# Performance work log

Measured on AMD Instinct MI355X. Metric: run time of the kernel, lower is better.

## Reference

```python
import jax, jax.numpy as jnp
import numpy as np
from math import sqrt


def setup_inputs() -> dict:
    key = jax.random.key(0)
    k1, k2, k3, k4, k5 = jax.random.split(key, 5)
    B, L, H, D = 16, 4096, 16, 64
    S, M = 4096, 256
    queries = jax.random.normal(k1, (B, L, H, D), dtype=jnp.float32)
    keys = jax.random.normal(k2, (B, S, H, D), dtype=jnp.float32)
    values = jax.random.normal(k3, (B, S, H, D), dtype=jnp.float32)
    # nn.Linear(L_k=S, M): weight [M, S], bias [M]
    squeeze_w = jax.random.normal(k4, (M, S), dtype=jnp.float32) / sqrt(S)
    squeeze_b = jax.random.normal(k5, (M,), dtype=jnp.float32) * 0.01
    return {"queries": queries, "keys": keys, "values": values,
            "squeeze_w": squeeze_w, "squeeze_b": squeeze_b}


def reference(queries, keys, values, squeeze_w, squeeze_b):
    # queries: [B,L,H,D]; keys/values: [B,S,H,D]; squeeze_w: [M,S]; squeeze_b: [M]
    B, L, H, D = queries.shape
    scale = 1.0 / sqrt(D)
    bias = squeeze_b[None, :, None, None]  # broadcast over [B,M,H,D]
    # Linear over the sequence axis S -> M (Linformer compression)
    keys_sq = jnp.einsum('bshd,ms->bmhd', keys, squeeze_w) + bias      # [B,M,H,D]
    values_sq = jnp.einsum('bshd,ms->bmhd', values, squeeze_w) + bias  # [B,M,H,D]
    # Scaled dot-product attention against compressed K/V
    attn = jnp.einsum('blhd,bmhd->bhlm', queries, keys_sq) * scale     # [B,H,L,M]
    attn = jax.nn.softmax(attn, axis=-1)  # dropout is identity in eval / p=0
    context = jnp.einsum('bhlm,bmhd->blhd', attn, values_sq)           # [B,L,H,D]
    return context
```

## Files before the change

kernel.cpp:

```cpp
#include <hip/hip_runtime.h>

#define NB 16
#define NL 4096
#define NH 16
#define ND 64
#define NS 4096
#define NM 256

typedef __fp16 f16;
typedef __attribute__((ext_vector_type(8)))  __fp16 f16x8;
typedef __attribute__((ext_vector_type(4)))  __fp16 f16x4;
typedef __attribute__((ext_vector_type(2)))  __fp16 f16x2;
typedef __attribute__((ext_vector_type(4)))  float  f32x4;
typedef __attribute__((ext_vector_type(16))) float  f32x16;

__device__ __forceinline__ void gload_lds16(const void* g, void* l) {
  __builtin_amdgcn_global_load_lds(
      (const __attribute__((address_space(1))) void*)g,
      (__attribute__((address_space(3))) void*)l, 16, 0, 0);
}

__device__ __forceinline__ int pk2(float a, float b) {
  f16x2 t = __builtin_amdgcn_cvt_pkrtz(a, b);
  union { f16x2 h; int i; } u; u.h = t; return u.i;
}

__global__ __launch_bounds__(256) void k_wcvt(const float* __restrict__ W,
                                              f16* __restrict__ Wk) {
  const int o  = blockIdx.x * 256 + threadIdx.x;
  const int m  = o & 255;
  const int kb = o >> 8;
  const float* src = W + (long)m * NS + kb * 8;
  f32x4 v0 = *(const f32x4*)(src);
  f32x4 v1 = *(const f32x4*)(src + 4);
  union { f16x8 v; f16x2 h2[4]; } pk;
  pk.h2[0] = __builtin_amdgcn_cvt_pkrtz(v0[0], v0[1]);
  pk.h2[1] = __builtin_amdgcn_cvt_pkrtz(v0[2], v0[3]);
  pk.h2[2] = __builtin_amdgcn_cvt_pkrtz(v1[0], v1[1]);
  pk.h2[3] = __builtin_amdgcn_cvt_pkrtz(v1[2], v1[3]);
  *(f16x8*)(Wk + (long)o * 8) = pk.v;
}

__global__ __launch_bounds__(512, 4) void k_squeeze(
    const f16* __restrict__ Wk, const float* __restrict__ keys,
    const float* __restrict__ values, const float* __restrict__ bias,
    f16* __restrict__ Ksq, f16* __restrict__ Vsq) {
  const int h = blockIdx.x & 15;
  const int b = (blockIdx.x >> 4) & 15;
  const int t = blockIdx.x >> 8;
  const float* __restrict__ X = t ? values : keys;

  __shared__ __align__(16) f16 XT0[64 * 72];
  __shared__ __align__(16) f16 XT1[64 * 72];

  const int tid  = threadIdx.x;
  const int lane = tid & 63;
  const int w    = tid >> 6;
  const int l31  = lane & 31;
  const int g    = lane >> 5;

  const int sp = tid & 31;
  const int ng = tid >> 5;
  const float* Xb = X + ((long)b * NS) * (NH * ND) + h * ND;

  f32x16 acc[2];
#pragma unroll
  for (int di = 0; di < 2; ++di)
#pragma unroll
    for (int r = 0; r < 16; ++r) acc[di][r] = 0.f;

  f32x4 xr[2];
#pragma unroll
  for (int r = 0; r < 2; ++r)
    xr[r] = *(const f32x4*)(Xb + (long)(2 * sp + r) * (NH * ND) + ng * 4);

  for (int kt = 0; kt < 64; ++kt) {
    f16* xt = (kt & 1) ? XT1 : XT0;
#pragma unroll
    for (int cc = 0; cc < 4; ++cc)
      *(int*)((char*)xt + (ng * 4 + cc) * 144 + sp * 4) = pk2(xr[0][cc], xr[1][cc]);
    __syncthreads();
    if (kt < 63) {
#pragma unroll
      for (int r = 0; r < 2; ++r)
        xr[r] = *(const f32x4*)(Xb + (long)((kt + 1) * 64 + 2 * sp + r) * (NH * ND) + ng * 4);
    }
#pragma unroll
    for (int ks = 0; ks < 4; ++ks) {
      const int kb = kt * 8 + ks * 2 + g;
      f16x8 af  = *(const f16x8*)(Wk + ((long)kb * 256 + w * 32 + l31) * 8);
      f16x8 bf0 = *(const f16x8*)((const char*)xt + l31 * 144 + ks * 32 + g * 16);
      f16x8 bf1 = *(const f16x8*)((const char*)xt + (32 + l31) * 144 + ks * 32 + g * 16);
      acc[0] = __builtin_amdgcn_mfma_f32_32x32x16_f16(af, bf0, acc[0], 0, 0, 0);
      acc[1] = __builtin_amdgcn_mfma_f32_32x32x16_f16(af, bf1, acc[1], 0, 0, 0);
    }
  }

  const long bh = b * 16 + h;
  if (t == 0) {
    f16* K = Ksq + bh * (NM * ND);
#pragma unroll
    for (int di = 0; di < 2; ++di)
#pragma unroll
      for (int r = 0; r < 16; ++r) {
        const int m = w * 32 + (r & 3) + 8 * (r >> 2) + 4 * g;
        const int d = di * 32 + l31;
        K[((d >> 3) * 256 + m) * 8 + (d & 7)] = (f16)(acc[di][r] + bias[m]);
      }
  } else {
    f16* V = Vsq + bh * (ND * NM);
#pragma unroll
    for (int di = 0; di < 2; ++di)
#pragma unroll
      for (int qq = 0; qq < 4; ++qq) {
        const int m0 = w * 32 + 8 * qq + 4 * g;
        const int d  = di * 32 + l31;
        f16x2 p0 = __builtin_amdgcn_cvt_pkrtz(acc[di][qq * 4 + 0] + bias[m0 + 0],
                                              acc[di][qq * 4 + 1] + bias[m0 + 1]);
        f16x2 p1 = __builtin_amdgcn_cvt_pkrtz(acc[di][qq * 4 + 2] + bias[m0 + 2],
                                              acc[di][qq * 4 + 3] + bias[m0 + 3]);
        f16x4 pv; pv[0] = p0[0]; pv[1] = p0[1]; pv[2] = p1[0]; pv[3] = p1[1];
        *(f16x4*)(V + ((m0 >> 3) * 64 + d) * 8 + 4 * g) = pv;
      }
  }
}

__global__ __launch_bounds__(256, 2) void k_attn(const float* __restrict__ Q,
                                                 const f16* __restrict__ Ksq,
                                                 const f16* __restrict__ Vsq,
                                                 float* __restrict__ Out) {
  const int xcd   = blockIdx.x & 7;
  const int local = blockIdx.x >> 3;
  const int bh    = xcd * 32 + (local >> 1);
  const int chunk = local & 1;
  const int b = bh >> 4, h = bh & 15;

  __shared__ __align__(16) f16 Klds[8 * 256 * 8];
  __shared__ __align__(16) f16 Vlds[32 * 64 * 8];

  const int tid = threadIdx.x, lane = tid & 63, w = tid >> 6;
  const int q = lane & 31, hi = lane >> 5;

  const float* Qlane = Q   + (((long)b * NL + q) * NH + h) * ND;
  float*       Olane = Out + (((long)b * NL + q) * NH + h) * ND;
  const float  c = 0.125f * 1.44269504088896f;

  f32x4 qv[8];
  {
    const float* qp = Qlane + (long)(chunk * 2048 + w * 32) * (NH * ND) + hi * 8;
#pragma unroll
    for (int kt = 0; kt < 4; ++kt) {
      qv[2 * kt]     = *(const f32x4*)(qp + kt * 16);
      qv[2 * kt + 1] = *(const f32x4*)(qp + kt * 16 + 4);
    }
  }

  {
    const f16* Kg = Ksq + (long)bh * 16384;
    const f16* Vg = Vsq + (long)bh * 16384;
#pragma unroll
    for (int i = 0; i < 8; ++i)
      gload_lds16(Kg + w * 4096 + i * 512 + lane * 8, (char*)Klds + w * 8192 + i * 1024);
#pragma unroll
    for (int i = 0; i < 8; ++i)
      gload_lds16(Vg + w * 4096 + i * 512 + lane * 8, (char*)Vlds + w * 8192 + i * 1024);
  }
  __syncthreads();

  for (int it = 0; it < 16; ++it) {
    const int row0 = chunk * 2048 + it * 128 + w * 32;

    union { f16x8 v; f16x2 h2[4]; } qb[4];
#pragma unroll
    for (int kt = 0; kt < 4; ++kt) {
      qb[kt].h2[0] = __builtin_amdgcn_cvt_pkrtz(qv[2 * kt][0], qv[2 * kt][1]);
      qb[kt].h2[1] = __builtin_amdgcn_cvt_pkrtz(qv[2 * kt][2], qv[2 * kt][3]);
      qb[kt].h2[2] = __builtin_amdgcn_cvt_pkrtz(qv[2 * kt + 1][0], qv[2 * kt + 1][1]);
      qb[kt].h2[3] = __builtin_amdgcn_cvt_pkrtz(qv[2 * kt + 1][2], qv[2 * kt + 1][3]);
    }

    if (it + 1 < 16) {
      const float* qp = Qlane + (long)(row0 + 128) * (NH * ND) + hi * 8;
#pragma unroll
      for (int kt = 0; kt < 4; ++kt) {
        qv[2 * kt]     = *(const f32x4*)(qp + kt * 16);
        qv[2 * kt + 1] = *(const f32x4*)(qp + kt * 16 + 4);
      }
    }

    f32x16 sa[8];
#pragma unroll
    for (int mf = 0; mf < 8; ++mf)
#pragma unroll
      for (int r = 0; r < 16; ++r) sa[mf][r] = 0.f;

#pragma unroll
    for (int kt = 0; kt < 4; ++kt) {
#pragma unroll
      for (int mf = 0; mf < 8; ++mf) {
        f16x8 ka = *(const f16x8*)((const char*)Klds +
                                   ((2 * kt + hi) * 256 + mf * 32 + q) * 16);
        sa[mf] = __builtin_amdgcn_mfma_f32_32x32x16_f16(ka, qb[kt].v, sa[mf], 0, 0, 0);
      }
    }

    f32x16 mm = sa[0];
#pragma unroll
    for (int mf = 1; mf < 8; ++mf)
#pragma unroll
      for (int r = 0; r < 16; ++r) mm[r] = fmaxf(mm[r], sa[mf][r]);
    float m8_0 = fmaxf(mm[0], mm[8]),  m8_1 = fmaxf(mm[1], mm[9]);
    float m8_2 = fmaxf(mm[2], mm[10]), m8_3 = fmaxf(mm[3], mm[11]);
    float m8_4 = fmaxf(mm[4], mm[12]), m8_5 = fmaxf(mm[5], mm[13]);
    float m8_6 = fmaxf(mm[6], mm[14]), m8_7 = fmaxf(mm[7], mm[15]);
    float mx = fmaxf(fmaxf(fmaxf(m8_0, m8_1), fmaxf(m8_2, m8_3)),
                     fmaxf(fmaxf(m8_4, m8_5), fmaxf(m8_6, m8_7)));
    mx = fmaxf(mx, __shfl_xor(mx, 32));

#pragma unroll
    for (int mf = 0; mf < 8; ++mf)
#pragma unroll
      for (int r = 0; r < 16; ++r)
        sa[mf][r] = __builtin_amdgcn_exp2f((sa[mf][r] - mx) * c);

    f32x16 t0 = sa[0] + sa[1];
    f32x16 t1 = sa[2] + sa[3];
    f32x16 t2 = sa[4] + sa[5];
    f32x16 t3 = sa[6] + sa[7];
    t0 = (t0 + t1) + (t2 + t3);
    float s8_0 = t0[0] + t0[8],  s8_1 = t0[1] + t0[9];
    float s8_2 = t0[2] + t0[10], s8_3 = t0[3] + t0[11];
    float s8_4 = t0[4] + t0[12], s8_5 = t0[5] + t0[13];
    float s8_6 = t0[6] + t0[14], s8_7 = t0[7] + t0[15];
    float sum = ((s8_0 + s8_1) + (s8_2 + s8_3)) + ((s8_4 + s8_5) + (s8_6 + s8_7));
    sum += __shfl_xor(sum, 32);
    const float inv = 1.0f / sum;

    f32x16 o[2];
#pragma unroll
    for (int df = 0; df < 2; ++df)
#pragma unroll
      for (int r = 0; r < 16; ++r) o[df][r] = 0.f;

#pragma unroll
    for (int t = 0; t < 16; ++t) {
      const int fp = t >> 1, s = t & 1;
      int a0 = pk2(sa[fp][8 * s + 0] * inv, sa[fp][8 * s + 1] * inv);
      int a1 = pk2(sa[fp][8 * s + 2] * inv, sa[fp][8 * s + 3] * inv);
      int b0 = pk2(sa[fp][8 * s + 4] * inv, sa[fp][8 * s + 5] * inv);
      int b1 = pk2(sa[fp][8 * s + 6] * inv, sa[fp][8 * s + 7] * inv);
      asm volatile("v_permlane32_swap_b32 %0, %1" : "+v"(a0), "+v"(b0));
      asm volatile("v_permlane32_swap_b32 %0, %1" : "+v"(a1), "+v"(b1));
      union { int w4[4]; f16x8 v; } pb;
      pb.w4[0] = a0; pb.w4[1] = a1; pb.w4[2] = b0; pb.w4[3] = b1;
#pragma unroll
      for (int df = 0; df < 2; ++df) {
        f16x8 va = *(const f16x8*)((const char*)Vlds +
                                   ((2 * t + hi) * 64 + df * 32 + q) * 16);
        o[df] = __builtin_amdgcn_mfma_f32_32x32x16_f16(va, pb.v, o[df], 0, 0, 0);
      }
    }

    float* op = Olane + (long)row0 * (NH * ND);
#pragma unroll
    for (int df = 0; df < 2; ++df)
#pragma unroll
      for (int rq = 0; rq < 4; ++rq) {
        f32x4 st;
        st[0] = o[df][rq * 4 + 0]; st[1] = o[df][rq * 4 + 1];
        st[2] = o[df][rq * 4 + 2]; st[3] = o[df][rq * 4 + 3];
        *(f32x4*)(op + df * 32 + rq * 8 + hi * 4) = st;
      }
  }
}

extern "C" void kernel_launch(void* const* d_in, const int* in_sizes, int n_in,
                              void* d_out, int out_size, void* d_ws, size_t ws_size,
                              hipStream_t stream) {
  const float* Qp   = (const float*)d_in[0];
  const float* Kp   = (const float*)d_in[1];
  const float* Vp   = (const float*)d_in[2];
  const float* Wp   = (const float*)d_in[3];
  const float* bp   = (const float*)d_in[4];
  float*       Outp = (float*)d_out;

  char* ws = (char*)d_ws;
  f16* Wk  = (f16*)ws;
  f16* Ksq = (f16*)(ws + (2l << 20));
  f16* Vsq = (f16*)(ws + (2l << 20) + (8l << 20));

  hipLaunchKernelGGL(k_wcvt, dim3(512), dim3(256), 0, stream, Wp, Wk);
  hipLaunchKernelGGL(k_squeeze, dim3(512), dim3(512), 0, stream, Wk, Kp, Vp, bp, Ksq, Vsq);
  hipLaunchKernelGGL(k_attn, dim3(512), dim3(256), 0, stream, Qp, Ksq, Vsq, Outp);
}
```

Before: 334.9 us.

## Load squeeze operands directly into registers, drop LDS staging and barriers

The squeeze kernel no longer stages the transposed K/V tile through shared memory with a barrier each step. Each lane now loads its B-fragment straight from global memory as scalar floats and packs them to fp16 in registers, with software double-buffering of both the X and W fragments. The wave layout also changes so each wave covers 64 m-rows by 32 d-columns instead of 32 by 64. This removes LDS traffic and synchronisation, at the cost of many strided scalar global loads (one float per row per lane) and poorer coalescing.

```diff
diff --git a/kernel.cpp b/kernel.cpp
--- a/kernel.cpp
+++ b/kernel.cpp
@@ -50,75 +50,93 @@
   const int t = blockIdx.x >> 8;
   const float* __restrict__ X = t ? values : keys;
 
-  __shared__ __align__(16) f16 XT0[64 * 72];
-  __shared__ __align__(16) f16 XT1[64 * 72];
-
-  const int tid  = threadIdx.x;
-  const int lane = tid & 63;
-  const int w    = tid >> 6;
+  const int lane = threadIdx.x & 63;
+  const int w    = threadIdx.x >> 6;
+  const int mq   = w & 3;
+  const int dh   = w >> 2;
   const int l31  = lane & 31;
   const int g    = lane >> 5;
 
-  const int sp = tid & 31;
-  const int ng = tid >> 5;
-  const float* Xb = X + ((long)b * NS) * (NH * ND) + h * ND;
+  const float* __restrict__ Xc =
+      X + ((long)b * NS) * (NH * ND) + h * ND + dh * 32 + l31;
+  const f16* __restrict__ Wl = Wk + ((long)(mq * 64) + l31) * 8;
 
   f32x16 acc[2];
 #pragma unroll
-  for (int di = 0; di < 2; ++di)
-#pragma unroll
-    for (int r = 0; r < 16; ++r) acc[di][r] = 0.f;
-
-  f32x4 xr[2];
-#pragma unroll
-  for (int r = 0; r < 2; ++r)
-    xr[r] = *(const f32x4*)(Xb + (long)(2 * sp + r) * (NH * ND) + ng * 4);
-
-  for (int kt = 0; kt < 64; ++kt) {
-    f16* xt = (kt & 1) ? XT1 : XT0;
-#pragma unroll
-    for (int cc = 0; cc < 4; ++cc)
-      *(int*)((char*)xt + (ng * 4 + cc) * 144 + sp * 4) = pk2(xr[0][cc], xr[1][cc]);
-    __syncthreads();
-    if (kt < 63) {
-#pragma unroll
-      for (int r = 0; r < 2; ++r)
-        xr[r] = *(const f32x4*)(Xb + (long)((kt + 1) * 64 + 2 * sp + r) * (NH * ND) + ng * 4);
-    }
-#pragma unroll
-    for (int ks = 0; ks < 4; ++ks) {
-      const int kb = kt * 8 + ks * 2 + g;
-      f16x8 af  = *(const f16x8*)(Wk + ((long)kb * 256 + w * 32 + l31) * 8);
-      f16x8 bf0 = *(const f16x8*)((const char*)xt + l31 * 144 + ks * 32 + g * 16);
-      f16x8 bf1 = *(const f16x8*)((const char*)xt + (32 + l31) * 144 + ks * 32 + g * 16);
-      acc[0] = __builtin_amdgcn_mfma_f32_32x32x16_f16(af, bf0, acc[0], 0, 0, 0);
-      acc[1] = __builtin_amdgcn_mfma_f32_32x32x16_f16(af, bf1, acc[1], 0, 0, 0);
-    }
-  }
+  for (int mf = 0; mf < 2; ++mf)
+#pragma unroll
+    for (int r = 0; r < 16; ++r) acc[mf][r] = 0.f;
+
+#define LD_X(dst, ks)                                                      \
+  {                                                                        \
+    const float* xp = Xc + ((long)(ks) * 16 + g * 8) * (NH * ND);          \
+    _Pragma("unroll") for (int j = 0; j < 8; ++j) dst[j] =                 \
+        xp[(long)j * (NH * ND)];                                           \
+  }
+#define LD_AF(dst, ks)                                                     \
+  {                                                                        \
+    const f16* wp = Wl + (((long)(ks) * 2 + g) * 256) * 8;                 \
+    dst[0] = *(const f16x8*)(wp);                                          \
+    dst[1] = *(const f16x8*)(wp + 32 * 8);                                 \
+  }
+
+  float xA[8], xB[8];
+  f16x8 afA[2], afB[2];
+  LD_X(xA, 0);
+  LD_X(xB, 1);
+  LD_AF(afA, 0);
+
+  for (int kt2 = 0; kt2 < 128; ++kt2) {
+    const int ks = 2 * kt2;
+    {
+      LD_AF(afB, ks + 1);
+      union { f16x8 v; f16x2 h2[4]; } bf;
+      bf.h2[0] = __builtin_amdgcn_cvt_pkrtz(xA[0], xA[1]);
+      bf.h2[1] = __builtin_amdgcn_cvt_pkrtz(xA[2], xA[3]);
+      bf.h2[2] = __builtin_amdgcn_cvt_pkrtz(xA[4], xA[5]);
+      bf.h2[3] = __builtin_amdgcn_cvt_pkrtz(xA[6], xA[7]);
+      if (kt2 < 127) LD_X(xA, ks + 2);
+      acc[0] = __builtin_amdgcn_mfma_f32_32x32x16_f16(afA[0], bf.v, acc[0], 0, 0, 0);
+      acc[1] = __builtin_amdgcn_mfma_f32_32x32x16_f16(afA[1], bf.v, acc[1], 0, 0, 0);
+    }
+    {
+      if (kt2 < 127) LD_AF(afA, ks + 2);
+      union { f16x8 v; f16x2 h2[4]; } bf;
+      bf.h2[0] = __builtin_amdgcn_cvt_pkrtz(xB[0], xB[1]);
+      bf.h2[1] = __builtin_amdgcn_cvt_pkrtz(xB[2], xB[3]);
+      bf.h2[2] = __builtin_amdgcn_cvt_pkrtz(xB[4], xB[5]);
+      bf.h2[3] = __builtin_amdgcn_cvt_pkrtz(xB[6], xB[7]);
+      if (kt2 < 127) LD_X(xB, ks + 3);
+      acc[0] = __builtin_amdgcn_mfma_f32_32x32x16_f16(afB[0], bf.v, acc[0], 0, 0, 0);
+      acc[1] = __builtin_amdgcn_mfma_f32_32x32x16_f16(afB[1], bf.v, acc[1], 0, 0, 0);
+    }
+  }
+#undef LD_X
+#undef LD_AF
 
   const long bh = b * 16 + h;
   if (t == 0) {
     f16* K = Ksq + bh * (NM * ND);
 #pragma unroll
-    for (int di = 0; di < 2; ++di)
+    for (int mf = 0; mf < 2; ++mf)
 #pragma unroll
       for (int r = 0; r < 16; ++r) {
-        const int m = w * 32 + (r & 3) + 8 * (r >> 2) + 4 * g;
-        const int d = di * 32 + l31;
-        K[((d >> 3) * 256 + m) * 8 + (d & 7)] = (f16)(acc[di][r] + bias[m]);
+        const int m = mq * 64 + mf * 32 + (r & 3) + 8 * (r >> 2) + 4 * g;
+        const int d = dh * 32 + l31;
+        K[((d >> 3) * 256 + m) * 8 + (d & 7)] = (f16)(acc[mf][r] + bias[m]);
       }
   } else {
     f16* V = Vsq + bh * (ND * NM);
 #pragma unroll
-    for (int di = 0; di < 2; ++di)
+    for (int mf = 0; mf < 2; ++mf)
 #pragma unroll
       for (int qq = 0; qq < 4; ++qq) {
-        const int m0 = w * 32 + 8 * qq + 4 * g;
-        const int d  = di * 32 + l31;
-        f16x2 p0 = __builtin_amdgcn_cvt_pkrtz(acc[di][qq * 4 + 0] + bias[m0 + 0],
-                                              acc[di][qq * 4 + 1] + bias[m0 + 1]);
-        f16x2 p1 = __builtin_amdgcn_cvt_pkrtz(acc[di][qq * 4 + 2] + bias[m0 + 2],
-                                              acc[di][qq * 4 + 3] + bias[m0 + 3]);
+        const int m0 = mq * 64 + mf * 32 + 8 * qq + 4 * g;
+        const int d  = dh * 32 + l31;
+        f16x2 p0 = __builtin_amdgcn_cvt_pkrtz(acc[mf][qq * 4 + 0] + bias[m0 + 0],
+                                              acc[mf][qq * 4 + 1] + bias[m0 + 1]);
+        f16x2 p1 = __builtin_amdgcn_cvt_pkrtz(acc[mf][qq * 4 + 2] + bias[m0 + 2],
+                                              acc[mf][qq * 4 + 3] + bias[m0 + 3]);
         f16x4 pv; pv[0] = p0[0]; pv[1] = p0[1]; pv[2] = p1[0]; pv[3] = p1[1];
         *(f16x4*)(V + ((m0 >> 3) * 64 + d) * 8 + 4 * g) = pv;
       }
@@ -287,7 +305,7 @@
   char* ws = (char*)d_ws;
   f16* Wk  = (f16*)ws;
   f16* Ksq = (f16*)(ws + (2l << 20));
-  f16* Vsq = (f16*)(ws + (2l << 20) + (8l << 20));
+  f16* Vsq = (f16*)(ws + (10l << 20));
 
   hipLaunchKernelGGL(k_wcvt, dim3(512), dim3(256), 0, stream, Wp, Wk);
   hipLaunchKernelGGL(k_squeeze, dim3(512), dim3(512), 0, stream, Wk, Kp, Vp, bp, Ksq, Vsq);
```

Measured after the change: 395.3 us. 18.1% more time.
